# Performance work log

Measured on AMD Instinct MI355X. Metric: run time of the kernel, lower is better.

The kernel has to match this reference:

```python
import jax, jax.numpy as jnp
import numpy as np

VLAD_K = 8   # vlad_cluster
GHOST_K = 2  # ghost_cluster
IN_DIM = 512
EPS = 1e-12  # F.normalize eps


def setup_inputs() -> dict:
    key = jax.random.key(0)
    k1, k2, k3, k4 = jax.random.split(key, 4)
    N, C, H, W = 32, IN_DIM, 16, 64
    KG = VLAD_K + GHOST_K
    x = jax.random.normal(k1, (N, C, H, W), dtype=jnp.float32)
    # 1x1 conv weight [KG, C, 1, 1] -> store as [KG, C]; bias [KG]
    conv_w = jax.random.normal(k2, (KG, C), dtype=jnp.float32) * (1.0 / np.sqrt(C))
    conv_b = jax.random.normal(k3, (KG,), dtype=jnp.float32) * 0.01
    centers = jax.random.uniform(k4, (KG, C), dtype=jnp.float32)
    return {"x": x, "conv_w": conv_w, "conv_b": conv_b, "centers": centers}


def reference(x, conv_w, conv_b, centers):
    N, C, H, W = x.shape
    P = H * W
    xf = x.reshape(N, C, P)                                   # [N,C,P]
    # 1x1 conv == per-position matmul over channels
    logits = jnp.einsum('ncp,kc->nkp', xf, conv_w) + conv_b[None, :, None]
    a = jax.nn.softmax(logits, axis=1)                        # softmax over clusters, [N,KG,P]
    # algebraic rewrite of sum_p a*(x - c): (a @ x^T) - (sum_p a) * c
    ax = jnp.einsum('nkp,ncp->nkc', a, xf)                    # [N,KG,C]
    a_sum = a.sum(axis=-1)                                    # [N,KG]
    cluster_res = ax - a_sum[..., None] * centers[None]       # [N,KG,C]
    cluster_res = cluster_res[:, :VLAD_K, :]                  # drop ghost clusters
    norm = jnp.linalg.norm(cluster_res, axis=-1, keepdims=True)
    cluster_res = cluster_res / jnp.maximum(norm, EPS)        # L2 normalize per cluster
    return cluster_res.reshape(N, VLAD_K * C)
```

## Files before the change

kernel.cpp:

```cpp
#include <hip/hip_runtime.h>
#include <math.h>

#define N_    32
#define C_    512
#define P_    1024
#define KG_   10
#define KV_   8
#define PBLK_ 64
#define NPB_  (P_ / PBLK_)
#define PS_   81

__global__ __launch_bounds__(512) void vlad_logits(
    const float* __restrict__ x, const float* __restrict__ w,
    const float* __restrict__ bias, float* __restrict__ a_ws,
    float* __restrict__ asum_blk) {
  __shared__ float part[PBLK_ * PS_];
  const int t  = threadIdx.x;
  const int pl = t & 63;
  const int cg = __builtin_amdgcn_readfirstlane(threadIdx.x >> 6);
  const int n  = blockIdx.x >> 4;
  const int pb = blockIdx.x & 15;
  const int p0 = pb * PBLK_;

  const float* xp = x + ((size_t)n * C_ + cg * 64) * P_ + p0 + pl;

  float acc[KG_];
#pragma unroll
  for (int k = 0; k < KG_; ++k) acc[k] = 0.f;

#pragma unroll 8
  for (int i = 0; i < 64; ++i) {
    const float xv = xp[(size_t)i * P_];
    const int c = cg * 64 + i;
#pragma unroll
    for (int k = 0; k < KG_; ++k) acc[k] += xv * w[k * C_ + c];
  }

#pragma unroll
  for (int k = 0; k < KG_; ++k) part[pl * PS_ + cg * KG_ + k] = acc[k];
  __syncthreads();

  if (t < 64) {
    float l[KG_];
    float m = -1e30f;
#pragma unroll
    for (int k = 0; k < KG_; ++k) {
      float s = bias[k];
#pragma unroll
      for (int g = 0; g < 8; ++g) s += part[t * PS_ + g * KG_ + k];
      l[k] = s;
      m = fmaxf(m, s);
    }
    float sum = 0.f;
#pragma unroll
    for (int k = 0; k < KG_; ++k) { l[k] = __expf(l[k] - m); sum += l[k]; }
    const float inv = 1.f / sum;
#pragma unroll
    for (int k = 0; k < KV_; ++k) {
      const float a = l[k] * inv;
      a_ws[((size_t)n * KV_ + k) * P_ + p0 + t] = a;
      float s = a;
      s += __shfl_xor(s, 1, 64);  s += __shfl_xor(s, 2, 64);
      s += __shfl_xor(s, 4, 64);  s += __shfl_xor(s, 8, 64);
      s += __shfl_xor(s, 16, 64); s += __shfl_xor(s, 32, 64);
      if (t == 0) asum_blk[(n * NPB_ + pb) * KV_ + k] = s;
    }
  }
}

__global__ __launch_bounds__(256) void vlad_ax(
    const float* __restrict__ x, const float* __restrict__ a_ws,
    float* __restrict__ ax_ws) {
  const int n    = blockIdx.x >> 5;
  const int cb   = blockIdx.x & 31;
  const int lane = threadIdx.x & 63;
  const int wv   = threadIdx.x >> 6;
  const int c0   = cb * 16 + wv * 4;

  const float* ap = a_ws + (size_t)n * KV_ * P_;
  const float* xp = x + (size_t)n * C_ * P_;

  float acc[4][8];
#pragma unroll
  for (int cc = 0; cc < 4; ++cc)
#pragma unroll
    for (int k = 0; k < 8; ++k) acc[cc][k] = 0.f;

#pragma unroll
  for (int i = 0; i < 4; ++i) {
    const int pb = i * 256 + lane * 4;
    float4 a4[8];
#pragma unroll
    for (int k = 0; k < 8; ++k)
      a4[k] = *reinterpret_cast<const float4*>(ap + (size_t)k * P_ + pb);
#pragma unroll
    for (int cc = 0; cc < 4; ++cc) {
      float4 x4 = *reinterpret_cast<const float4*>(xp + (size_t)(c0 + cc) * P_ + pb);
#pragma unroll
      for (int k = 0; k < 8; ++k)
        acc[cc][k] += x4.x * a4[k].x + x4.y * a4[k].y
                    + x4.z * a4[k].z + x4.w * a4[k].w;
    }
  }

  float v[32];
#pragma unroll
  for (int cc = 0; cc < 4; ++cc)
#pragma unroll
    for (int k = 0; k < 8; ++k) v[cc * 8 + k] = acc[cc][k];

  {
    const bool hi = lane & 1;
#pragma unroll
    for (int j = 0; j < 16; ++j) {
      float send = hi ? v[j] : v[j + 16];
      float keep = hi ? v[j + 16] : v[j];
      v[j] = keep + __shfl_xor(send, 1, 64);
    }
  }
  {
    const bool hi = lane & 2;
#pragma unroll
    for (int j = 0; j < 8; ++j) {
      float send = hi ? v[j] : v[j + 8];
      float keep = hi ? v[j + 8] : v[j];
      v[j] = keep + __shfl_xor(send, 2, 64);
    }
  }
  {
    const bool hi = lane & 4;
#pragma unroll
    for (int j = 0; j < 4; ++j) {
      float send = hi ? v[j] : v[j + 4];
      float keep = hi ? v[j + 4] : v[j];
      v[j] = keep + __shfl_xor(send, 4, 64);
    }
  }
  {
    const bool hi = lane & 8;
#pragma unroll
    for (int j = 0; j < 2; ++j) {
      float send = hi ? v[j] : v[j + 2];
      float keep = hi ? v[j + 2] : v[j];
      v[j] = keep + __shfl_xor(send, 8, 64);
    }
  }
  {
    const bool hi = lane & 16;
    float send = hi ? v[0] : v[1];
    float keep = hi ? v[1] : v[0];
    v[0] = keep + __shfl_xor(send, 16, 64);
  }
  v[0] += __shfl_xor(v[0], 32, 64);

  if (lane < 32) {
    const int o = ((lane & 1) << 4) | ((lane & 2) << 2) | (lane & 4)
                | (((lane >> 3) & 1) << 1) | ((lane >> 4) & 1);
    const int cc = o >> 3;
    const int k  = o & 7;
    ax_ws[((size_t)n * KV_ + k) * C_ + (c0 + cc)] = v[0];
  }
}

__global__ __launch_bounds__(256) void vlad_fin(
    const float* __restrict__ ax_ws, const float* __restrict__ asum_blk,
    const float* __restrict__ centers, float* __restrict__ out) {
  __shared__ float sred[4];
  const int n = blockIdx.x >> 3;
  const int k = blockIdx.x & 7;
  const int t = threadIdx.x, lane = t & 63, wv = t >> 6;

  float asv = 0.f;
#pragma unroll
  for (int pb = 0; pb < NPB_; ++pb)
    asv += asum_blk[(n * NPB_ + pb) * KV_ + k];

  const int c = t * 2;
  const float2 av = *reinterpret_cast<const float2*>(&ax_ws[((size_t)n * KV_ + k) * C_ + c]);
  const float2 ct = *reinterpret_cast<const float2*>(&centers[k * C_ + c]);
  const float r0 = av.x - asv * ct.x;
  const float r1 = av.y - asv * ct.y;

  float ss = r0 * r0 + r1 * r1;
#pragma unroll
  for (int d = 1; d < 64; d <<= 1) ss += __shfl_xor(ss, d, 64);
  if (lane == 0) sred[wv] = ss;
  __syncthreads();
  const float tot = (sred[0] + sred[1]) + (sred[2] + sred[3]);
  const float inv = 1.f / fmaxf(sqrtf(tot), 1e-12f);

  out[(size_t)n * (KV_ * C_) + k * C_ + c]     = r0 * inv;
  out[(size_t)n * (KV_ * C_) + k * C_ + c + 1] = r1 * inv;
}

extern "C" void kernel_launch(void* const* d_in, const int* in_sizes, int n_in,
                              void* d_out, int out_size, void* d_ws, size_t ws_size,
                              hipStream_t stream) {
  const float* x       = (const float*)d_in[0];
  const float* conv_w  = (const float*)d_in[1];
  const float* conv_b  = (const float*)d_in[2];
  const float* centers = (const float*)d_in[3];
  float* out = (float*)d_out;

  float* a_ws     = (float*)d_ws;
  float* ax_ws    = a_ws + (size_t)N_ * KV_ * P_;
  float* asum_blk = ax_ws + (size_t)N_ * KV_ * C_;

  hipLaunchKernelGGL(vlad_logits, dim3(N_ * NPB_), dim3(512), 0, stream,
                     x, conv_w, conv_b, a_ws, asum_blk);
  hipLaunchKernelGGL(vlad_ax,     dim3(N_ * 32),   dim3(256), 0, stream,
                     x, a_ws, ax_ws);
  hipLaunchKernelGGL(vlad_fin,    dim3(N_ * KV_),  dim3(256), 0, stream,
                     ax_ws, asum_blk, centers, out);
}
```

Before: 117.6 us.

## Fuse softmax-assignment and aggregation kernels, keeping assignments in LDS with atomics

```diff
diff --git a/kernel.cpp b/kernel.cpp
--- a/kernel.cpp
+++ b/kernel.cpp
@@ -10,11 +10,12 @@
 #define NPB_  (P_ / PBLK_)
 #define PS_   81
 
-__global__ __launch_bounds__(512) void vlad_logits(
+__global__ __launch_bounds__(512) void vlad_fused(
     const float* __restrict__ x, const float* __restrict__ w,
-    const float* __restrict__ bias, float* __restrict__ a_ws,
+    const float* __restrict__ bias, float* __restrict__ ax_ws,
     float* __restrict__ asum_blk) {
   __shared__ float part[PBLK_ * PS_];
+  __shared__ float a_lds[KV_][64];
   const int t  = threadIdx.x;
   const int pl = t & 63;
   const int cg = __builtin_amdgcn_readfirstlane(threadIdx.x >> 6);
@@ -58,7 +59,7 @@
 #pragma unroll
     for (int k = 0; k < KV_; ++k) {
       const float a = l[k] * inv;
-      a_ws[((size_t)n * KV_ + k) * P_ + p0 + t] = a;
+      a_lds[k][t] = a;
       float s = a;
       s += __shfl_xor(s, 1, 64);  s += __shfl_xor(s, 2, 64);
       s += __shfl_xor(s, 4, 64);  s += __shfl_xor(s, 8, 64);
@@ -66,99 +67,65 @@
       if (t == 0) asum_blk[(n * NPB_ + pb) * KV_ + k] = s;
     }
   }
-}
+  __syncthreads();
 
-__global__ __launch_bounds__(256) void vlad_ax(
-    const float* __restrict__ x, const float* __restrict__ a_ws,
-    float* __restrict__ ax_ws) {
-  const int n    = blockIdx.x >> 5;
-  const int cb   = blockIdx.x & 31;
-  const int lane = threadIdx.x & 63;
-  const int wv   = threadIdx.x >> 6;
-  const int c0   = cb * 16 + wv * 4;
+  float ak[KV_];
+#pragma unroll
+  for (int k = 0; k < KV_; ++k) ak[k] = a_lds[k][pl];
 
-  const float* ap = a_ws + (size_t)n * KV_ * P_;
-  const float* xp = x + (size_t)n * C_ * P_;
+  const float* xq = x + (size_t)n * C_ * P_ + p0 + pl;
+  float* axn = ax_ws + (size_t)n * KV_ * C_;
 
-  float acc[4][8];
+  const bool h1 = pl & 1, h2 = pl & 2, h4 = pl & 4, h8 = pl & 8, h16 = pl & 16;
+  const int o = ((pl & 1) << 4) | ((pl & 2) << 2) | (pl & 4)
+              | (((pl >> 3) & 1) << 1) | ((pl >> 4) & 1);
+  const int occ = o >> 3;
+  const int ok  = o & 7;
+
+#pragma unroll 2
+  for (int q = 0; q < 16; ++q) {
+    const int c0 = cg * 64 + q * 4;
+    float v[32];
 #pragma unroll
-  for (int cc = 0; cc < 4; ++cc)
+    for (int cc = 0; cc < 4; ++cc) {
+      const float xv = xq[(size_t)(c0 + cc) * P_];
 #pragma unroll
-    for (int k = 0; k < 8; ++k) acc[cc][k] = 0.f;
+      for (int k = 0; k < 8; ++k) v[cc * 8 + k] = xv * ak[k];
+    }
 
 #pragma unroll
-  for (int i = 0; i < 4; ++i) {
-    const int pb = i * 256 + lane * 4;
-    float4 a4[8];
-#pragma unroll
-    for (int k = 0; k < 8; ++k)
-      a4[k] = *reinterpret_cast<const float4*>(ap + (size_t)k * P_ + pb);
-#pragma unroll
-    for (int cc = 0; cc < 4; ++cc) {
-      float4 x4 = *reinterpret_cast<const float4*>(xp + (size_t)(c0 + cc) * P_ + pb);
-#pragma unroll
-      for (int k = 0; k < 8; ++k)
-        acc[cc][k] += x4.x * a4[k].x + x4.y * a4[k].y
-                    + x4.z * a4[k].z + x4.w * a4[k].w;
-    }
-  }
-
-  float v[32];
-#pragma unroll
-  for (int cc = 0; cc < 4; ++cc)
-#pragma unroll
-    for (int k = 0; k < 8; ++k) v[cc * 8 + k] = acc[cc][k];
-
-  {
-    const bool hi = lane & 1;
-#pragma unroll
     for (int j = 0; j < 16; ++j) {
-      float send = hi ? v[j] : v[j + 16];
-      float keep = hi ? v[j + 16] : v[j];
+      float send = h1 ? v[j] : v[j + 16];
+      float keep = h1 ? v[j + 16] : v[j];
       v[j] = keep + __shfl_xor(send, 1, 64);
     }
-  }
-  {
-    const bool hi = lane & 2;
 #pragma unroll
     for (int j = 0; j < 8; ++j) {
-      float send = hi ? v[j] : v[j + 8];
-      float keep = hi ? v[j + 8] : v[j];
+      float send = h2 ? v[j] : v[j + 8];
+      float keep = h2 ? v[j + 8] : v[j];
       v[j] = keep + __shfl_xor(send, 2, 64);
     }
-  }
-  {
-    const bool hi = lane & 4;
 #pragma unroll
     for (int j = 0; j < 4; ++j) {
-      float send = hi ? v[j] : v[j + 4];
-      float keep = hi ? v[j + 4] : v[j];
+      float send = h4 ? v[j] : v[j + 4];
+      float keep = h4 ? v[j + 4] : v[j];
       v[j] = keep + __shfl_xor(send, 4, 64);
     }
-  }
-  {
-    const bool hi = lane & 8;
 #pragma unroll
     for (int j = 0; j < 2; ++j) {
-      float send = hi ? v[j] : v[j + 2];
-      float keep = hi ? v[j + 2] : v[j];
+      float send = h8 ? v[j] : v[j + 2];
+      float keep = h8 ? v[j + 2] : v[j];
       v[j] = keep + __shfl_xor(send, 8, 64);
     }
-  }
-  {
-    const bool hi = lane & 16;
-    float send = hi ? v[0] : v[1];
-    float keep = hi ? v[1] : v[0];
-    v[0] = keep + __shfl_xor(send, 16, 64);
-  }
-  v[0] += __shfl_xor(v[0], 32, 64);
+    {
+      float send = h16 ? v[0] : v[1];
+      float keep = h16 ? v[1] : v[0];
+      v[0] = keep + __shfl_xor(send, 16, 64);
+    }
+    v[0] += __shfl_xor(v[0], 32, 64);
 
-  if (lane < 32) {
-    const int o = ((lane & 1) << 4) | ((lane & 2) << 2) | (lane & 4)
-                | (((lane >> 3) & 1) << 1) | ((lane >> 4) & 1);
-    const int cc = o >> 3;
-    const int k  = o & 7;
-    ax_ws[((size_t)n * KV_ + k) * C_ + (c0 + cc)] = v[0];
+    if (pl < 32)
+      atomicAdd(&axn[ok * C_ + c0 + occ], v[0]);
   }
 }
 
@@ -202,14 +169,12 @@
   const float* centers = (const float*)d_in[3];
   float* out = (float*)d_out;
 
-  float* a_ws     = (float*)d_ws;
-  float* ax_ws    = a_ws + (size_t)N_ * KV_ * P_;
+  float* ax_ws    = (float*)d_ws;
   float* asum_blk = ax_ws + (size_t)N_ * KV_ * C_;
 
-  hipLaunchKernelGGL(vlad_logits, dim3(N_ * NPB_), dim3(512), 0, stream,
-                     x, conv_w, conv_b, a_ws, asum_blk);
-  hipLaunchKernelGGL(vlad_ax,     dim3(N_ * 32),   dim3(256), 0, stream,
-                     x, a_ws, ax_ws);
-  hipLaunchKernelGGL(vlad_fin,    dim3(N_ * KV_),  dim3(256), 0, stream,
+  hipMemsetAsync(ax_ws, 0, (size_t)N_ * KV_ * C_ * sizeof(float), stream);
+  hipLaunchKernelGGL(vlad_fused, dim3(N_ * NPB_), dim3(512), 0, stream,
+                     x, conv_w, conv_b, ax_ws, asum_blk);
+  hipLaunchKernelGGL(vlad_fin,   dim3(N_ * KV_),  dim3(256), 0, stream,
                      ax_ws, asum_blk, centers, out);
 }
```

Result: slower. 132.0 us (+12.2%).
